# Kernel tuning notes

Measured on AMD Instinct MI355X. Metric: run time of the kernel, lower is better.

## Reference

```python
import jax, jax.numpy as jnp
import numpy as np

N = 100000   # nodes per type
E = 400000   # edges per relation
D = 128      # in_dim == out_dim
H = 4        # heads
DK = D // H  # 32
EPS = 1e-5


def setup_inputs() -> dict:
    key = jax.random.key(0)
    ks = jax.random.split(key, 16)
    s = 1.0 / np.sqrt(D)  # fan-in scaling for stable activations
    inp = {
        "x_drug": jax.random.normal(ks[0], (N, D), jnp.float32),
        "x_dis": jax.random.normal(ks[1], (N, D), jnp.float32),
        "Wp_drug": jax.random.normal(ks[2], (D, D), jnp.float32) * s,
        "bp_drug": jnp.zeros((D,), jnp.float32),
        "Wp_dis": jax.random.normal(ks[3], (D, D), jnp.float32) * s,
        "bp_dis": jnp.zeros((D,), jnp.float32),
        "Wk_r0": jax.random.normal(ks[4], (D, D), jnp.float32) * s,
        "Wv_r0": jax.random.normal(ks[5], (D, D), jnp.float32) * s,
        "Wk_r1": jax.random.normal(ks[6], (D, D), jnp.float32) * s,
        "Wv_r1": jax.random.normal(ks[7], (D, D), jnp.float32) * s,
        "Wu_drug": jax.random.normal(ks[8], (D, D), jnp.float32) * s,
        "bu_drug": jnp.zeros((D,), jnp.float32),
        "Wu_dis": jax.random.normal(ks[9], (D, D), jnp.float32) * s,
        "bu_dis": jnp.zeros((D,), jnp.float32),
        "g_drug": jnp.ones((D,), jnp.float32),
        "be_drug": jnp.zeros((D,), jnp.float32),
        "g_dis": jnp.ones((D,), jnp.float32),
        "be_dis": jnp.zeros((D,), jnp.float32),
        "ei_r0": jax.random.randint(ks[10], (2, E), 0, N, jnp.int32),  # drug -> dis
        "ei_r1": jax.random.randint(ks[11], (2, E), 0, N, jnp.int32),  # dis  -> drug
    }
    return inp


def _rel_attention(h_src_all, h_dst_all, ei, Wk, Wv, n_dst):
    # gather -> per-relation K/V proj -> edge softmax over dst -> scatter-add
    src, dst = ei[0], ei[1]
    h_src = h_src_all[src]                                  # [E, D]
    Q = h_dst_all[dst].reshape(-1, H, DK)                   # [E, H, DK]
    K = (h_src @ Wk).reshape(-1, H, DK)
    V = (h_src @ Wv).reshape(-1, H, DK)
    scores = jnp.sum(Q * K, axis=-1) / np.sqrt(DK)          # [E, H]
    # scatter_softmax over destination groups (numerically stable)
    m = jax.lax.stop_gradient(
        jax.ops.segment_max(scores, dst, num_segments=n_dst))  # [N, H]
    ex = jnp.exp(scores - m[dst])
    ssum = jax.ops.segment_sum(ex, dst, num_segments=n_dst)    # [N, H]
    attn = ex / ssum[dst]                                      # [E, H]
    wV = (V * attn[..., None]).reshape(-1, D)                  # [E, D]
    return jax.ops.segment_sum(wV, dst, num_segments=n_dst)    # [N, D]


def _update(h, agg, Wu, bu, g, be):
    x = h + (agg @ Wu + bu)  # skip + update (dropout=0)
    mu = jnp.mean(x, axis=-1, keepdims=True)
    var = jnp.var(x, axis=-1, keepdims=True)
    ln = (x - mu) * jax.lax.rsqrt(var + EPS) * g + be
    return jax.nn.relu(ln)


def reference(x_drug, x_dis, Wp_drug, bp_drug, Wp_dis, bp_dis,
              Wk_r0, Wv_r0, Wk_r1, Wv_r1,
              Wu_drug, bu_drug, Wu_dis, bu_dis,
              g_drug, be_drug, g_dis, be_dis, ei_r0, ei_r1):
    # type-specific projection
    h_drug = x_drug @ Wp_drug + bp_drug
    h_dis = x_dis @ Wp_dis + bp_dis
    # per-relation attention + intra/inter-type aggregation
    agg_dis = _rel_attention(h_drug, h_dis, ei_r0, Wk_r0, Wv_r0, N)
    agg_drug = _rel_attention(h_dis, h_drug, ei_r1, Wk_r1, Wv_r1, N)
    out_drug = _update(h_drug, agg_drug, Wu_drug, bu_drug, g_drug, be_drug)
    out_dis = _update(h_dis, agg_dis, Wu_dis, bu_dis, g_dis, be_dis)
    return jnp.stack([out_drug, out_dis])  # [2, N, D]
```

## Files before the change

kernel.cpp:

```cpp
#include <hip/hip_runtime.h>
#include <math.h>

#define NN 100000
#define EE 400000
#define DD 128

typedef __attribute__((ext_vector_type(8))) short bf16x8;
typedef __attribute__((ext_vector_type(4))) float f32x4;

__device__ __forceinline__ unsigned short f2bf(float f) {
  unsigned u = __float_as_uint(f);
  u += 0x7FFF + ((u >> 16) & 1);
  return (unsigned short)(u >> 16);
}
__device__ __forceinline__ float bf2f(unsigned short u) {
  return __uint_as_float(((unsigned)u) << 16);
}

__global__ __launch_bounds__(256) void prep_weights(
    const float* __restrict__ Wp_dr, const float* __restrict__ bp_dr,
    const float* __restrict__ Wp_di, const float* __restrict__ bp_di,
    const float* __restrict__ Wu_dr, const float* __restrict__ Wu_di,
    const float* __restrict__ Bk0, const float* __restrict__ Bv0,
    const float* __restrict__ Bk1, const float* __restrict__ Bv1,
    unsigned short* __restrict__ Wpt_dr, unsigned short* __restrict__ Wpt_di,
    unsigned short* __restrict__ Wut_dr, unsigned short* __restrict__ Wut_di,
    unsigned short* __restrict__ Wkt0, float* __restrict__ bk0,
    unsigned short* __restrict__ Wvt0, float* __restrict__ bv0,
    unsigned short* __restrict__ Wkt1, float* __restrict__ bk1,
    unsigned short* __restrict__ Wvt1, float* __restrict__ bv1) {
  const int b = blockIdx.x, t = threadIdx.x;
  if (b < 256) {
    const int id = b * 256 + t;
    const int m = id >> 14, rem = id & 16383, k = rem & 127, c = rem >> 7;
    const float* W = (m == 0) ? Wp_dr : (m == 1) ? Wp_di : (m == 2) ? Wu_dr : Wu_di;
    unsigned short* O = (m == 0) ? Wpt_dr : (m == 1) ? Wpt_di : (m == 2) ? Wut_dr : Wut_di;
    O[c * DD + k] = f2bf(W[(size_t)k * DD + c]);
  } else if (b < 512) {
    const int id = (b - 256) * 256 + t;
    const int m = id >> 14, rem = id & 16383, k = rem & 127, c = rem >> 7;
    const float* A = (m < 2) ? Wp_dr : Wp_di;
    const float* B = (m == 0) ? Bk0 : (m == 1) ? Bv0 : (m == 2) ? Bk1 : Bv1;
    unsigned short* O = (m == 0) ? Wkt0 : (m == 1) ? Wvt0 : (m == 2) ? Wkt1 : Wvt1;
    const float4* a4 = (const float4*)(A + (size_t)k * DD);
    float s = 0.0f;
#pragma unroll 8
    for (int j4 = 0; j4 < 32; ++j4) {
      const float4 av = a4[j4];
      s += av.x * B[(4 * j4 + 0) * DD + c] + av.y * B[(4 * j4 + 1) * DD + c]
         + av.z * B[(4 * j4 + 2) * DD + c] + av.w * B[(4 * j4 + 3) * DD + c];
    }
    O[c * DD + k] = f2bf(s);
  } else {
    const int id = (b - 512) * 256 + t;
    if (id < 512) {
      const int m = id >> 7, c = id & 127;
      const float* bp = (m < 2) ? bp_dr : bp_di;
      const float* B = (m == 0) ? Bk0 : (m == 1) ? Bv0 : (m == 2) ? Bk1 : Bv1;
      float* bo = (m == 0) ? bk0 : (m == 1) ? bv0 : (m == 2) ? bk1 : bv1;
      float s = 0.0f;
#pragma unroll 8
      for (int j = 0; j < DD; ++j) s += bp[j] * B[j * DD + c];
      bo[c] = s;
    }
  }
}

#define STAGE_W(SRC)                                                          \
  do {                                                                        \
    __syncthreads();                                                          \
    _Pragma("unroll") for (int i_ = threadIdx.x; i_ < 2048; i_ += 256) {      \
      const int L_ = i_ * 16;                                                 \
      *(float4*)((char*)WL + (L_ ^ (((L_ >> 8) & 7) << 4))) =                 \
          ((const float4*)(SRC))[i_];                                         \
    }                                                                         \
    __syncthreads();                                                          \
  } while (0)

__device__ __forceinline__ void mfma_tile_store(
    const unsigned short* WL, const bf16x8* a, int lane, int rowbase,
    bool wvalid, const float* __restrict__ bias, float* __restrict__ outf,
    unsigned short* __restrict__ outb) {
  const int r0 = rowbase + (lane >> 4) * 4;
#pragma unroll
  for (int ni = 0; ni < 8; ++ni) {
    const int cl = ni * 16 + (lane & 15);
    f32x4 acc = {0.f, 0.f, 0.f, 0.f};
#pragma unroll
    for (int kk = 0; kk < 4; ++kk) {
      int boff = cl * 256 + kk * 64 + (lane >> 4) * 16;
      boff ^= (cl & 7) << 4;
      const bf16x8 bb = *(const bf16x8*)((const char*)WL + boff);
      acc = __builtin_amdgcn_mfma_f32_16x16x32_bf16(a[kk], bb, acc, 0, 0, 0);
    }
    if (wvalid) {
      const float bv = bias[cl];
      if (outf) {
#pragma unroll
        for (int r = 0; r < 4; ++r)
          outf[(size_t)(r0 + r) * DD + cl] = acc[r] + bv;
      } else {
#pragma unroll
        for (int r = 0; r < 4; ++r)
          outb[(size_t)(r0 + r) * DD + cl] = f2bf(acc[r] + bv);
      }
    }
  }
}

__global__ __launch_bounds__(256) void fused_proj(
    const float* __restrict__ x0, const unsigned short* __restrict__ Wpt0,
    const float* __restrict__ bp0, const unsigned short* __restrict__ Wkta,
    const float* __restrict__ bka, const unsigned short* __restrict__ Wvta,
    const float* __restrict__ bva, float* __restrict__ h0,
    unsigned short* __restrict__ K0, unsigned short* __restrict__ V0,
    const float* __restrict__ x1, const unsigned short* __restrict__ Wpt1,
    const float* __restrict__ bp1, const unsigned short* __restrict__ Wktb,
    const float* __restrict__ bkb, const unsigned short* __restrict__ Wvtb,
    const float* __restrict__ bvb, float* __restrict__ h1,
    unsigned short* __restrict__ K1, unsigned short* __restrict__ V1, int half) {
  __shared__ unsigned short WL[DD * DD];
  int bid = blockIdx.x;
  const bool second = bid >= half;
  if (second) bid -= half;
  const float* x = second ? x1 : x0;
  const unsigned short* Wpt = second ? Wpt1 : Wpt0;
  const float* bpv = second ? bp1 : bp0;
  const unsigned short* Wkt = second ? Wktb : Wkta;
  const float* bkv = second ? bkb : bka;
  const unsigned short* Wvt = second ? Wvtb : Wvta;
  const float* bvv = second ? bvb : bva;
  float* h = second ? h1 : h0;
  unsigned short* K = second ? K1 : K0;
  unsigned short* V = second ? V1 : V0;

  const int tid = threadIdx.x, lane = tid & 63, wid = tid >> 6;
  const int rowbase = bid * 64 + wid * 16;
  const bool wvalid = rowbase < NN;
  bf16x8 a[4];
  if (wvalid) {
    const int arow = rowbase + (lane & 15);
    const float* xr = x + (size_t)arow * DD + (lane >> 4) * 8;
#pragma unroll
    for (int kk = 0; kk < 4; ++kk) {
      const float4 f0 = *(const float4*)(xr + kk * 32);
      const float4 f1 = *(const float4*)(xr + kk * 32 + 4);
      a[kk][0] = (short)f2bf(f0.x); a[kk][1] = (short)f2bf(f0.y);
      a[kk][2] = (short)f2bf(f0.z); a[kk][3] = (short)f2bf(f0.w);
      a[kk][4] = (short)f2bf(f1.x); a[kk][5] = (short)f2bf(f1.y);
      a[kk][6] = (short)f2bf(f1.z); a[kk][7] = (short)f2bf(f1.w);
    }
  } else {
#pragma unroll
    for (int kk = 0; kk < 4; ++kk)
#pragma unroll
      for (int j = 0; j < 8; ++j) a[kk][j] = 0;
  }
  STAGE_W(Wpt);
  mfma_tile_store(WL, a, lane, rowbase, wvalid, bpv, h, nullptr);
  STAGE_W(Wkt);
  mfma_tile_store(WL, a, lane, rowbase, wvalid, bkv, nullptr, K);
  STAGE_W(Wvt);
  mfma_tile_store(WL, a, lane, rowbase, wvalid, bvv, nullptr, V);
}

__global__ __launch_bounds__(256) void update_ln2(
    const float* __restrict__ ha, const unsigned short* __restrict__ agga,
    const unsigned short* __restrict__ Wuta, const float* __restrict__ bua,
    const float* __restrict__ ga, const float* __restrict__ bea,
    float* __restrict__ outa,
    const float* __restrict__ hb, const unsigned short* __restrict__ aggb,
    const unsigned short* __restrict__ Wutb, const float* __restrict__ bub,
    const float* __restrict__ gb, const float* __restrict__ beb,
    float* __restrict__ outb, int half) {
  __shared__ unsigned short WL[DD * DD];
  int bid = blockIdx.x;
  const bool second = bid >= half;
  if (second) bid -= half;
  const float* h = second ? hb : ha;
  const unsigned short* agg = second ? aggb : agga;
  const unsigned short* Wut = second ? Wutb : Wuta;
  const float* bu = second ? bub : bua;
  const float* g = second ? gb : ga;
  const float* be = second ? beb : bea;
  float* out = second ? outb : outa;

  const int tid = threadIdx.x, lane = tid & 63, wid = tid >> 6;
  const int rowbase = bid * 64 + wid * 16;
  const bool wvalid = rowbase < NN;
  bf16x8 a[4];
  if (wvalid) {
    const int arow = rowbase + (lane & 15);
#pragma unroll
    for (int kk = 0; kk < 4; ++kk)
      a[kk] = *(const bf16x8*)(agg + (size_t)arow * DD + kk * 32 + (lane >> 4) * 8);
  } else {
#pragma unroll
    for (int kk = 0; kk < 4; ++kk)
#pragma unroll
      for (int j = 0; j < 8; ++j) a[kk][j] = 0;
  }
  STAGE_W(Wut);
  f32x4 acc[8];
  const int r0 = rowbase + (lane >> 4) * 4;
#pragma unroll
  for (int ni = 0; ni < 8; ++ni) {
    const int cl = ni * 16 + (lane & 15);
    acc[ni] = (f32x4){0.f, 0.f, 0.f, 0.f};
#pragma unroll
    for (int kk = 0; kk < 4; ++kk) {
      int boff = cl * 256 + kk * 64 + (lane >> 4) * 16;
      boff ^= (cl & 7) << 4;
      const bf16x8 bb = *(const bf16x8*)((const char*)WL + boff);
      acc[ni] = __builtin_amdgcn_mfma_f32_16x16x32_bf16(a[kk], bb, acc[ni], 0, 0, 0);
    }
  }
  if (!wvalid) return;
#pragma unroll
  for (int ni = 0; ni < 8; ++ni) {
    const int cl = ni * 16 + (lane & 15);
    const float bv = bu[cl];
#pragma unroll
    for (int r = 0; r < 4; ++r)
      acc[ni][r] += h[(size_t)(r0 + r) * DD + cl] + bv;
  }
  float mean[4], inv[4];
#pragma unroll
  for (int r = 0; r < 4; ++r) {
    float s = 0.f, q = 0.f;
#pragma unroll
    for (int ni = 0; ni < 8; ++ni) {
      const float v = acc[ni][r];
      s += v; q += v * v;
    }
    s += __shfl_xor(s, 1); q += __shfl_xor(q, 1);
    s += __shfl_xor(s, 2); q += __shfl_xor(q, 2);
    s += __shfl_xor(s, 4); q += __shfl_xor(q, 4);
    s += __shfl_xor(s, 8); q += __shfl_xor(q, 8);
    const float mu = s * (1.0f / 128.0f);
    mean[r] = mu;
    inv[r] = rsqrtf(q * (1.0f / 128.0f) - mu * mu + 1e-5f);
  }
#pragma unroll
  for (int ni = 0; ni < 8; ++ni) {
    const int cl = ni * 16 + (lane & 15);
    const float gv = g[cl], bev = be[cl];
#pragma unroll
    for (int r = 0; r < 4; ++r)
      out[(size_t)(r0 + r) * DD + cl] =
          fmaxf((acc[ni][r] - mean[r]) * inv[r] * gv + bev, 0.0f);
  }
}

__global__ __launch_bounds__(256) void count_deg2(const int* __restrict__ ei0,
                                                  const int* __restrict__ ei1,
                                                  int* __restrict__ deg) {
  const int e = blockIdx.x * 256 + threadIdx.x;
  if (e >= 2 * EE) return;
  const int d = (e < EE) ? ei0[EE + e] : (NN + ei1[e]);
  atomicAdd(&deg[d], 1);
}

__global__ __launch_bounds__(256) void scan1(const int* __restrict__ deg,
                                             int* __restrict__ excl,
                                             int* __restrict__ partials, int n) {
  __shared__ int ls[256];
  const int b0 = blockIdx.x * 1024;
  const int t = threadIdx.x;
  int v[4];
  int s = 0;
#pragma unroll
  for (int i = 0; i < 4; ++i) {
    const int idx = b0 + t * 4 + i;
    v[i] = (idx < n) ? deg[idx] : 0;
    s += v[i];
  }
  ls[t] = s;
  __syncthreads();
  for (int off = 1; off < 256; off <<= 1) {
    const int x = (t >= off) ? ls[t - off] : 0;
    __syncthreads();
    ls[t] += x;
    __syncthreads();
  }
  int ex = ls[t] - s;
#pragma unroll
  for (int i = 0; i < 4; ++i) {
    const int idx = b0 + t * 4 + i;
    if (idx < n) excl[idx] = ex;
    ex += v[i];
  }
  if (t == 255) partials[blockIdx.x] = ls[255];
}

__global__ __launch_bounds__(256) void scan2(int* __restrict__ partials, int nb) {
  __shared__ int ls[256];
  const int t = threadIdx.x;
  const int v = (t < nb) ? partials[t] : 0;
  ls[t] = v;
  __syncthreads();
  for (int off = 1; off < 256; off <<= 1) {
    const int x = (t >= off) ? ls[t - off] : 0;
    __syncthreads();
    ls[t] += x;
    __syncthreads();
  }
  if (t < nb) partials[t] = ls[t] - v;
}

__global__ __launch_bounds__(256) void scan3(const int* __restrict__ excl,
                                             const int* __restrict__ partials,
                                             int n, int* __restrict__ rowptr,
                                             int* __restrict__ cursor) {
  const int i = blockIdx.x * 256 + threadIdx.x;
  if (i < n) {
    const int v = excl[i] + partials[i >> 10];
    rowptr[i] = v;
    cursor[i] = v;
  }
  if (i == 0) rowptr[n] = 2 * EE;
}

__global__ __launch_bounds__(256) void fill_csr2(const int* __restrict__ ei0,
                                                 const int* __restrict__ ei1,
                                                 int* __restrict__ cursor,
                                                 int* __restrict__ csr_src) {
  const int e = blockIdx.x * 256 + threadIdx.x;
  if (e >= 2 * EE) return;
  int s, d;
  if (e < EE) { s = ei0[e]; d = ei0[EE + e]; }
  else        { s = ei1[e - EE]; d = NN + ei1[e]; }
  const int p = atomicAdd(&cursor[d], 1);
  csr_src[p] = s;
}

__global__ __launch_bounds__(256) void dst_attention(
    const float* __restrict__ Hq0, const unsigned short* __restrict__ K0,
    const unsigned short* __restrict__ V0, unsigned short* __restrict__ agg0,
    const float* __restrict__ Hq1, const unsigned short* __restrict__ K1,
    const unsigned short* __restrict__ V1, unsigned short* __restrict__ agg1,
    const int* __restrict__ rowptr, const int* __restrict__ csr_src) {
  const int gw = blockIdx.x * 4 + (threadIdx.x >> 6);
  if (gw >= 2 * NN) return;
  const bool rel1 = gw >= NN;
  const int node = rel1 ? gw - NN : gw;
  const float* Hq = rel1 ? Hq1 : Hq0;
  const unsigned short* K = rel1 ? K1 : K0;
  const unsigned short* V = rel1 ? V1 : V0;
  unsigned short* agg = rel1 ? agg1 : agg0;

  const int lane = threadIdx.x & 63;
  const int sub = lane & 15;
  const int grp = lane >> 4;
  const int beg = rowptr[gw], end = rowptr[gw + 1];
  const float4* qp = (const float4*)(Hq + (size_t)node * DD + sub * 8);
  const float4 q0 = qp[0], q1 = qp[1];
  float av[8] = {0.f, 0.f, 0.f, 0.f, 0.f, 0.f, 0.f, 0.f};
  float lsum = 0.0f;
  for (int i = beg + grp; i < end; i += 4) {
    const int sidx = csr_src[i];
    const uint4 kp = *(const uint4*)(K + (size_t)sidx * DD + sub * 8);
    float p;
    p  = q0.x * __uint_as_float(kp.x << 16);
    p += q0.y * __uint_as_float(kp.x & 0xFFFF0000u);
    p += q0.z * __uint_as_float(kp.y << 16);
    p += q0.w * __uint_as_float(kp.y & 0xFFFF0000u);
    p += q1.x * __uint_as_float(kp.z << 16);
    p += q1.y * __uint_as_float(kp.z & 0xFFFF0000u);
    p += q1.z * __uint_as_float(kp.w << 16);
    p += q1.w * __uint_as_float(kp.w & 0xFFFF0000u);
    p += __shfl_xor(p, 1);
    p += __shfl_xor(p, 2);
    const float wgt = __expf(p * 0.17677669529663689f);
    const uint4 vp = *(const uint4*)(V + (size_t)sidx * DD + sub * 8);
    lsum += wgt;
    av[0] += wgt * __uint_as_float(vp.x << 16);
    av[1] += wgt * __uint_as_float(vp.x & 0xFFFF0000u);
    av[2] += wgt * __uint_as_float(vp.y << 16);
    av[3] += wgt * __uint_as_float(vp.y & 0xFFFF0000u);
    av[4] += wgt * __uint_as_float(vp.z << 16);
    av[5] += wgt * __uint_as_float(vp.z & 0xFFFF0000u);
    av[6] += wgt * __uint_as_float(vp.w << 16);
    av[7] += wgt * __uint_as_float(vp.w & 0xFFFF0000u);
  }
#pragma unroll
  for (int d = 0; d < 8; ++d) {
    av[d] += __shfl_xor(av[d], 16);
    av[d] += __shfl_xor(av[d], 32);
  }
  lsum += __shfl_xor(lsum, 16);
  lsum += __shfl_xor(lsum, 32);
  if (grp == 0) {
    const float invl = (lsum > 0.0f) ? (1.0f / lsum) : 0.0f;
    uint4 o;
    o.x = (unsigned)f2bf(av[0] * invl) | ((unsigned)f2bf(av[1] * invl) << 16);
    o.y = (unsigned)f2bf(av[2] * invl) | ((unsigned)f2bf(av[3] * invl) << 16);
    o.z = (unsigned)f2bf(av[4] * invl) | ((unsigned)f2bf(av[5] * invl) << 16);
    o.w = (unsigned)f2bf(av[6] * invl) | ((unsigned)f2bf(av[7] * invl) << 16);
    *(uint4*)(agg + (size_t)node * DD + sub * 8) = o;
  }
}

extern "C" void kernel_launch(void* const* d_in, const int* in_sizes, int n_in,
                              void* d_out, int out_size, void* d_ws, size_t ws_size,
                              hipStream_t stream) {
  const float* x_drug  = (const float*)d_in[0];
  const float* x_dis   = (const float*)d_in[1];
  const float* Wp_drug = (const float*)d_in[2];
  const float* bp_drug = (const float*)d_in[3];
  const float* Wp_dis  = (const float*)d_in[4];
  const float* bp_dis  = (const float*)d_in[5];
  const float* Wk_r0   = (const float*)d_in[6];
  const float* Wv_r0   = (const float*)d_in[7];
  const float* Wk_r1   = (const float*)d_in[8];
  const float* Wv_r1   = (const float*)d_in[9];
  const float* Wu_drug = (const float*)d_in[10];
  const float* bu_drug = (const float*)d_in[11];
  const float* Wu_dis  = (const float*)d_in[12];
  const float* bu_dis  = (const float*)d_in[13];
  const float* g_drug  = (const float*)d_in[14];
  const float* be_drug = (const float*)d_in[15];
  const float* g_dis   = (const float*)d_in[16];
  const float* be_dis  = (const float*)d_in[17];
  const int* ei_r0     = (const int*)d_in[18];
  const int* ei_r1     = (const int*)d_in[19];

  float* out = (float*)d_out;
  float* h_drug = out;
  float* h_dis  = out + (size_t)NN * DD;

  const size_t ND = (size_t)NN * DD;
  char* w = (char*)d_ws;
  unsigned short* Kr0  = (unsigned short*)w; w += ND * 2;
  unsigned short* Vr0  = (unsigned short*)w; w += ND * 2;
  unsigned short* Kr1  = (unsigned short*)w; w += ND * 2;
  unsigned short* Vr1  = (unsigned short*)w; w += ND * 2;
  unsigned short* agdr = (unsigned short*)w; w += ND * 2;
  unsigned short* agdi = (unsigned short*)w; w += ND * 2;
  unsigned short* Wpt_dr = (unsigned short*)w; w += DD * DD * 2;
  unsigned short* Wpt_di = (unsigned short*)w; w += DD * DD * 2;
  unsigned short* Wut_dr = (unsigned short*)w; w += DD * DD * 2;
  unsigned short* Wut_di = (unsigned short*)w; w += DD * DD * 2;
  unsigned short* Wkt0 = (unsigned short*)w; w += DD * DD * 2;
  unsigned short* Wvt0 = (unsigned short*)w; w += DD * DD * 2;
  unsigned short* Wkt1 = (unsigned short*)w; w += DD * DD * 2;
  unsigned short* Wvt1 = (unsigned short*)w; w += DD * DD * 2;
  float* bk0 = (float*)w; w += DD * 4;
  float* bv0 = (float*)w; w += DD * 4;
  float* bk1 = (float*)w; w += DD * 4;
  float* bv1 = (float*)w; w += DD * 4;
  int* deg      = (int*)w; w += 2 * NN * 4;
  int* excl     = (int*)w; w += 2 * NN * 4;
  int* rowptr   = (int*)w; w += (2 * NN + 1) * 4;
  int* cursor   = (int*)w; w += 2 * NN * 4;
  int* partials = (int*)w; w += 256 * 4;
  int* csr_src  = (int*)w; w += 2 * EE * 4;

  const int gemm_blocks = (NN + 63) / 64;
  const int edge_blocks2 = (2 * EE + 255) / 256;
  const int nchunks = (2 * NN + 1023) / 1024;
  const int n256 = (2 * NN + 255) / 256;
  const int attn_blocks = (2 * NN + 3) / 4;
  dim3 b256(256);

  prep_weights<<<514, b256, 0, stream>>>(
      Wp_drug, bp_drug, Wp_dis, bp_dis, Wu_drug, Wu_dis,
      Wk_r0, Wv_r0, Wk_r1, Wv_r1,
      Wpt_dr, Wpt_di, Wut_dr, Wut_di,
      Wkt0, bk0, Wvt0, bv0, Wkt1, bk1, Wvt1, bv1);

  fused_proj<<<2 * gemm_blocks, b256, 0, stream>>>(
      x_drug, Wpt_dr, bp_drug, Wkt0, bk0, Wvt0, bv0, h_drug, Kr0, Vr0,
      x_dis,  Wpt_di, bp_dis,  Wkt1, bk1, Wvt1, bv1, h_dis,  Kr1, Vr1,
      gemm_blocks);

  hipMemsetAsync(deg, 0, 2 * NN * sizeof(int), stream);
  count_deg2<<<edge_blocks2, b256, 0, stream>>>(ei_r0, ei_r1, deg);
  scan1<<<nchunks, b256, 0, stream>>>(deg, excl, partials, 2 * NN);
  scan2<<<1, b256, 0, stream>>>(partials, nchunks);
  scan3<<<n256, b256, 0, stream>>>(excl, partials, 2 * NN, rowptr, cursor);
  fill_csr2<<<edge_blocks2, b256, 0, stream>>>(ei_r0, ei_r1, cursor, csr_src);

  dst_attention<<<attn_blocks, b256, 0, stream>>>(
      h_dis, Kr0, Vr0, agdi,
      h_drug, Kr1, Vr1, agdr,
      rowptr, csr_src);

  update_ln2<<<2 * gemm_blocks, b256, 0, stream>>>(
      h_drug, agdr, Wut_dr, bu_drug, g_drug, be_drug, h_drug,
      h_dis,  agdi, Wut_di, bu_dis,  g_dis,  be_dis,  h_dis,
      gemm_blocks);
}
```

Before: 316.1 us.

## Store projected h in bf16 and stage GEMM tiles through LDS for coalesced I/O

The projected node features h are now written as a bf16 workspace buffer instead of fp32 in the output, which halves their write traffic and the reads made by attention and update. The GEMM kernels now stage input rows and output tiles through shared memory so global loads and stores are full-row coalesced vectors. The attention query dot product uses the bf16 fdot2 builtin when it is available. In exchange the kernels use more LDS, which may lower occupancy, and h loses precision before the residual add.

```diff
diff --git a/kernel.cpp b/kernel.cpp
--- a/kernel.cpp
+++ b/kernel.cpp
@@ -7,6 +7,13 @@
 
 typedef __attribute__((ext_vector_type(8))) short bf16x8;
 typedef __attribute__((ext_vector_type(4))) float f32x4;
+
+#if defined(__has_builtin)
+#if __has_builtin(__builtin_amdgcn_fdot2_f32_bf16)
+#define HAVE_FDOT2 1
+typedef __attribute__((ext_vector_type(2))) __bf16 bf16x2t;
+#endif
+#endif
 
 __device__ __forceinline__ unsigned short f2bf(float f) {
   unsigned u = __float_as_uint(f);
@@ -66,22 +73,19 @@
   }
 }
 
-#define STAGE_W(SRC)                                                          \
-  do {                                                                        \
-    __syncthreads();                                                          \
-    _Pragma("unroll") for (int i_ = threadIdx.x; i_ < 2048; i_ += 256) {      \
-      const int L_ = i_ * 16;                                                 \
-      *(float4*)((char*)WL + (L_ ^ (((L_ >> 8) & 7) << 4))) =                 \
-          ((const float4*)(SRC))[i_];                                         \
-    }                                                                         \
-    __syncthreads();                                                          \
-  } while (0)
-
-__device__ __forceinline__ void mfma_tile_store(
-    const unsigned short* WL, const bf16x8* a, int lane, int rowbase,
-    bool wvalid, const float* __restrict__ bias, float* __restrict__ outf,
-    unsigned short* __restrict__ outb) {
-  const int r0 = rowbase + (lane >> 4) * 4;
+__device__ __forceinline__ void proj_phase(
+    const unsigned short* __restrict__ Wt, const float* __restrict__ bias,
+    unsigned short* __restrict__ outg, unsigned short* WL, unsigned short* OT,
+    const bf16x8* a, int tid, int lane, int wid, int rb) {
+  __syncthreads();
+#pragma unroll
+  for (int i = tid; i < 2048; i += 256) {
+    const int L = i * 16;
+    *(float4*)((char*)WL + (L ^ (((L >> 8) & 7) << 4))) = ((const float4*)Wt)[i];
+  }
+  __syncthreads();
+  const int lr0 = (lane >> 4) * 4;
+  const int trow = wid * 16 + lr0;
 #pragma unroll
   for (int ni = 0; ni < 8; ++ni) {
     const int cl = ni * 16 + (lane & 15);
@@ -93,18 +97,17 @@
       const bf16x8 bb = *(const bf16x8*)((const char*)WL + boff);
       acc = __builtin_amdgcn_mfma_f32_16x16x32_bf16(a[kk], bb, acc, 0, 0, 0);
     }
-    if (wvalid) {
-      const float bv = bias[cl];
-      if (outf) {
-#pragma unroll
-        for (int r = 0; r < 4; ++r)
-          outf[(size_t)(r0 + r) * DD + cl] = acc[r] + bv;
-      } else {
-#pragma unroll
-        for (int r = 0; r < 4; ++r)
-          outb[(size_t)(r0 + r) * DD + cl] = f2bf(acc[r] + bv);
-      }
-    }
+    const float bv = bias[cl];
+#pragma unroll
+    for (int r = 0; r < 4; ++r)
+      OT[(trow + r) * DD + cl] = f2bf(acc[r] + bv);
+  }
+  __syncthreads();
+#pragma unroll
+  for (int it = 0; it < 4; ++it) {
+    const int row = it * 16 + (tid >> 4), c = (tid & 15) * 8;
+    if (rb + row < NN)
+      *(uint4*)(outg + (size_t)(rb + row) * DD + c) = *(const uint4*)(OT + row * DD + c);
   }
 }
 
@@ -112,14 +115,16 @@
     const float* __restrict__ x0, const unsigned short* __restrict__ Wpt0,
     const float* __restrict__ bp0, const unsigned short* __restrict__ Wkta,
     const float* __restrict__ bka, const unsigned short* __restrict__ Wvta,
-    const float* __restrict__ bva, float* __restrict__ h0,
+    const float* __restrict__ bva, unsigned short* __restrict__ h0,
     unsigned short* __restrict__ K0, unsigned short* __restrict__ V0,
     const float* __restrict__ x1, const unsigned short* __restrict__ Wpt1,
     const float* __restrict__ bp1, const unsigned short* __restrict__ Wktb,
     const float* __restrict__ bkb, const unsigned short* __restrict__ Wvtb,
-    const float* __restrict__ bvb, float* __restrict__ h1,
+    const float* __restrict__ bvb, unsigned short* __restrict__ h1,
     unsigned short* __restrict__ K1, unsigned short* __restrict__ V1, int half) {
   __shared__ unsigned short WL[DD * DD];
+  __shared__ unsigned short AL[64 * DD];
+  __shared__ unsigned short OT[64 * DD];
   int bid = blockIdx.x;
   const bool second = bid >= half;
   if (second) bid -= half;
@@ -130,79 +135,98 @@
   const float* bkv = second ? bkb : bka;
   const unsigned short* Wvt = second ? Wvtb : Wvta;
   const float* bvv = second ? bvb : bva;
-  float* h = second ? h1 : h0;
+  unsigned short* h = second ? h1 : h0;
   unsigned short* K = second ? K1 : K0;
   unsigned short* V = second ? V1 : V0;
 
   const int tid = threadIdx.x, lane = tid & 63, wid = tid >> 6;
-  const int rowbase = bid * 64 + wid * 16;
-  const bool wvalid = rowbase < NN;
+  const int rb = bid * 64;
+#pragma unroll
+  for (int it = 0; it < 8; ++it) {
+    const int r = it * 8 + (tid >> 5), c = (tid & 31) * 4;
+    unsigned long long pk = 0;
+    if (rb + r < NN) {
+      const float4 f = *(const float4*)(x + (size_t)(rb + r) * DD + c);
+      pk = (unsigned long long)f2bf(f.x) | ((unsigned long long)f2bf(f.y) << 16)
+         | ((unsigned long long)f2bf(f.z) << 32) | ((unsigned long long)f2bf(f.w) << 48);
+    }
+    int L = r * 256 + c * 2;
+    L ^= (r & 7) << 4;
+    *(unsigned long long*)((char*)AL + L) = pk;
+  }
+  __syncthreads();
   bf16x8 a[4];
-  if (wvalid) {
-    const int arow = rowbase + (lane & 15);
-    const float* xr = x + (size_t)arow * DD + (lane >> 4) * 8;
+  {
+    const int ar = wid * 16 + (lane & 15);
 #pragma unroll
     for (int kk = 0; kk < 4; ++kk) {
-      const float4 f0 = *(const float4*)(xr + kk * 32);
-      const float4 f1 = *(const float4*)(xr + kk * 32 + 4);
-      a[kk][0] = (short)f2bf(f0.x); a[kk][1] = (short)f2bf(f0.y);
-      a[kk][2] = (short)f2bf(f0.z); a[kk][3] = (short)f2bf(f0.w);
-      a[kk][4] = (short)f2bf(f1.x); a[kk][5] = (short)f2bf(f1.y);
-      a[kk][6] = (short)f2bf(f1.z); a[kk][7] = (short)f2bf(f1.w);
-    }
-  } else {
-#pragma unroll
-    for (int kk = 0; kk < 4; ++kk)
-#pragma unroll
-      for (int j = 0; j < 8; ++j) a[kk][j] = 0;
-  }
-  STAGE_W(Wpt);
-  mfma_tile_store(WL, a, lane, rowbase, wvalid, bpv, h, nullptr);
-  STAGE_W(Wkt);
-  mfma_tile_store(WL, a, lane, rowbase, wvalid, bkv, nullptr, K);
-  STAGE_W(Wvt);
-  mfma_tile_store(WL, a, lane, rowbase, wvalid, bvv, nullptr, V);
+      int L = ar * 256 + kk * 64 + (lane >> 4) * 16;
+      L ^= (ar & 7) << 4;
+      a[kk] = *(const bf16x8*)((const char*)AL + L);
+    }
+  }
+  proj_phase(Wpt, bpv, h, WL, OT, a, tid, lane, wid, rb);
+  proj_phase(Wkt, bkv, K, WL, OT, a, tid, lane, wid, rb);
+  proj_phase(Wvt, bvv, V, WL, OT, a, tid, lane, wid, rb);
 }
 
 __global__ __launch_bounds__(256) void update_ln2(
-    const float* __restrict__ ha, const unsigned short* __restrict__ agga,
-    const unsigned short* __restrict__ Wuta, const float* __restrict__ bua,
-    const float* __restrict__ ga, const float* __restrict__ bea,
-    float* __restrict__ outa,
-    const float* __restrict__ hb, const unsigned short* __restrict__ aggb,
-    const unsigned short* __restrict__ Wutb, const float* __restrict__ bub,
-    const float* __restrict__ gb, const float* __restrict__ beb,
-    float* __restrict__ outb, int half) {
+    const unsigned short* __restrict__ hA, const unsigned short* __restrict__ aggA,
+    const unsigned short* __restrict__ WutA, const float* __restrict__ buA,
+    const float* __restrict__ gA, const float* __restrict__ beA,
+    float* __restrict__ outA,
+    const unsigned short* __restrict__ hB, const unsigned short* __restrict__ aggB,
+    const unsigned short* __restrict__ WutB, const float* __restrict__ buB,
+    const float* __restrict__ gB, const float* __restrict__ beB,
+    float* __restrict__ outB, int half) {
   __shared__ unsigned short WL[DD * DD];
+  __shared__ unsigned short AL[64 * DD];
+  __shared__ unsigned short OT[64 * DD];
   int bid = blockIdx.x;
   const bool second = bid >= half;
   if (second) bid -= half;
-  const float* h = second ? hb : ha;
-  const unsigned short* agg = second ? aggb : agga;
-  const unsigned short* Wut = second ? Wutb : Wuta;
-  const float* bu = second ? bub : bua;
-  const float* g = second ? gb : ga;
-  const float* be = second ? beb : bea;
-  float* out = second ? outb : outa;
+  const unsigned short* h = second ? hB : hA;
+  const unsigned short* agg = second ? aggB : aggA;
+  const unsigned short* Wut = second ? WutB : WutA;
+  const float* bu = second ? buB : buA;
+  const float* g = second ? gB : gA;
+  const float* be = second ? beB : beA;
+  float* out = second ? outB : outA;
 
   const int tid = threadIdx.x, lane = tid & 63, wid = tid >> 6;
-  const int rowbase = bid * 64 + wid * 16;
-  const bool wvalid = rowbase < NN;
+  const int rb = bid * 64;
+#pragma unroll
+  for (int it = 0; it < 4; ++it) {
+    const int row = it * 16 + (tid >> 4), c = (tid & 15) * 8;
+    uint4 va = {0, 0, 0, 0}, vh = {0, 0, 0, 0};
+    if (rb + row < NN) {
+      va = *(const uint4*)(agg + (size_t)(rb + row) * DD + c);
+      vh = *(const uint4*)(h + (size_t)(rb + row) * DD + c);
+    }
+    int L = row * 256 + c * 2;
+    L ^= (row & 7) << 4;
+    *(uint4*)((char*)AL + L) = va;
+    *(uint4*)(OT + row * DD + c) = vh;
+  }
+#pragma unroll
+  for (int i = tid; i < 2048; i += 256) {
+    const int L = i * 16;
+    *(float4*)((char*)WL + (L ^ (((L >> 8) & 7) << 4))) = ((const float4*)Wut)[i];
+  }
+  __syncthreads();
   bf16x8 a[4];
-  if (wvalid) {
-    const int arow = rowbase + (lane & 15);
-#pragma unroll
-    for (int kk = 0; kk < 4; ++kk)
-      a[kk] = *(const bf16x8*)(agg + (size_t)arow * DD + kk * 32 + (lane >> 4) * 8);
-  } else {
-#pragma unroll
-    for (int kk = 0; kk < 4; ++kk)
-#pragma unroll
-      for (int j = 0; j < 8; ++j) a[kk][j] = 0;
-  }
-  STAGE_W(Wut);
+  {
+    const int ar = wid * 16 + (lane & 15);
+#pragma unroll
+    for (int kk = 0; kk < 4; ++kk) {
+      int L = ar * 256 + kk * 64 + (lane >> 4) * 16;
+      L ^= (ar & 7) << 4;
+      a[kk] = *(const bf16x8*)((const char*)AL + L);
+    }
+  }
   f32x4 acc[8];
-  const int r0 = rowbase + (lane >> 4) * 4;
+  const int lr0 = (lane >> 4) * 4;
+  const int trow = wid * 16 + lr0;
 #pragma unroll
   for (int ni = 0; ni < 8; ++ni) {
     const int cl = ni * 16 + (lane & 15);
@@ -215,14 +239,13 @@
       acc[ni] = __builtin_amdgcn_mfma_f32_16x16x32_bf16(a[kk], bb, acc[ni], 0, 0, 0);
     }
   }
-  if (!wvalid) return;
 #pragma unroll
   for (int ni = 0; ni < 8; ++ni) {
     const int cl = ni * 16 + (lane & 15);
     const float bv = bu[cl];
 #pragma unroll
     for (int r = 0; r < 4; ++r)
-      acc[ni][r] += h[(size_t)(r0 + r) * DD + cl] + bv;
+      acc[ni][r] += bf2f(OT[(trow + r) * DD + cl]) + bv;
   }
   float mean[4], inv[4];
 #pragma unroll
@@ -241,14 +264,23 @@
     mean[r] = mu;
     inv[r] = rsqrtf(q * (1.0f / 128.0f) - mu * mu + 1e-5f);
   }
+  __syncthreads();
+  float* WLf = (float*)WL;
 #pragma unroll
   for (int ni = 0; ni < 8; ++ni) {
     const int cl = ni * 16 + (lane & 15);
     const float gv = g[cl], bev = be[cl];
 #pragma unroll
     for (int r = 0; r < 4; ++r)
-      out[(size_t)(r0 + r) * DD + cl] =
+      WLf[(trow + r) * DD + cl] =
           fmaxf((acc[ni][r] - mean[r]) * inv[r] * gv + bev, 0.0f);
+  }
+  __syncthreads();
+#pragma unroll
+  for (int it = 0; it < 8; ++it) {
+    const int row = it * 8 + (tid >> 5), c = (tid & 31) * 4;
+    if (rb + row < NN)
+      *(float4*)(out + (size_t)(rb + row) * DD + c) = *(const float4*)(WLf + row * DD + c);
   }
 }
 
@@ -335,16 +367,16 @@
 }
 
 __global__ __launch_bounds__(256) void dst_attention(
-    const float* __restrict__ Hq0, const unsigned short* __restrict__ K0,
+    const unsigned short* __restrict__ Hq0, const unsigned short* __restrict__ K0,
     const unsigned short* __restrict__ V0, unsigned short* __restrict__ agg0,
-    const float* __restrict__ Hq1, const unsigned short* __restrict__ K1,
+    const unsigned short* __restrict__ Hq1, const unsigned short* __restrict__ K1,
     const unsigned short* __restrict__ V1, unsigned short* __restrict__ agg1,
     const int* __restrict__ rowptr, const int* __restrict__ csr_src) {
   const int gw = blockIdx.x * 4 + (threadIdx.x >> 6);
   if (gw >= 2 * NN) return;
   const bool rel1 = gw >= NN;
   const int node = rel1 ? gw - NN : gw;
-  const float* Hq = rel1 ? Hq1 : Hq0;
+  const unsigned short* Hq = rel1 ? Hq1 : Hq0;
   const unsigned short* K = rel1 ? K1 : K0;
   const unsigned short* V = rel1 ? V1 : V0;
   unsigned short* agg = rel1 ? agg1 : agg0;
@@ -353,22 +385,36 @@
   const int sub = lane & 15;
   const int grp = lane >> 4;
   const int beg = rowptr[gw], end = rowptr[gw + 1];
-  const float4* qp = (const float4*)(Hq + (size_t)node * DD + sub * 8);
-  const float4 q0 = qp[0], q1 = qp[1];
+  const uint4 qu = *(const uint4*)(Hq + (size_t)node * DD + sub * 8);
+#if defined(HAVE_FDOT2)
+  const bf16x2t q0 = __builtin_bit_cast(bf16x2t, qu.x);
+  const bf16x2t q1 = __builtin_bit_cast(bf16x2t, qu.y);
+  const bf16x2t q2 = __builtin_bit_cast(bf16x2t, qu.z);
+  const bf16x2t q3 = __builtin_bit_cast(bf16x2t, qu.w);
+#else
+  float qf[8];
+  qf[0] = bf2f((unsigned short)qu.x); qf[1] = bf2f((unsigned short)(qu.x >> 16));
+  qf[2] = bf2f((unsigned short)qu.y); qf[3] = bf2f((unsigned short)(qu.y >> 16));
+  qf[4] = bf2f((unsigned short)qu.z); qf[5] = bf2f((unsigned short)(qu.z >> 16));
+  qf[6] = bf2f((unsigned short)qu.w); qf[7] = bf2f((unsigned short)(qu.w >> 16));
+#endif
   float av[8] = {0.f, 0.f, 0.f, 0.f, 0.f, 0.f, 0.f, 0.f};
   float lsum = 0.0f;
   for (int i = beg + grp; i < end; i += 4) {
     const int sidx = csr_src[i];
     const uint4 kp = *(const uint4*)(K + (size_t)sidx * DD + sub * 8);
+#if defined(HAVE_FDOT2)
+    float p = __builtin_amdgcn_fdot2_f32_bf16(__builtin_bit_cast(bf16x2t, kp.x), q0, 0.0f, false);
+    p = __builtin_amdgcn_fdot2_f32_bf16(__builtin_bit_cast(bf16x2t, kp.y), q1, p, false);
+    p = __builtin_amdgcn_fdot2_f32_bf16(__builtin_bit_cast(bf16x2t, kp.z), q2, p, false);
+    p = __builtin_amdgcn_fdot2_f32_bf16(__builtin_bit_cast(bf16x2t, kp.w), q3, p, false);
+#else
     float p;
-    p  = q0.x * __uint_as_float(kp.x << 16);
-    p += q0.y * __uint_as_float(kp.x & 0xFFFF0000u);
-    p += q0.z * __uint_as_float(kp.y << 16);
-    p += q0.w * __uint_as_float(kp.y & 0xFFFF0000u);
-    p += q1.x * __uint_as_float(kp.z << 16);
-    p += q1.y * __uint_as_float(kp.z & 0xFFFF0000u);
-    p += q1.z * __uint_as_float(kp.w << 16);
-    p += q1.w * __uint_as_float(kp.w & 0xFFFF0000u);
+    p  = qf[0] * bf2f((unsigned short)kp.x) + qf[1] * bf2f((unsigned short)(kp.x >> 16));
+    p += qf[2] * bf2f((unsigned short)kp.y) + qf[3] * bf2f((unsigned short)(kp.y >> 16));
+    p += qf[4] * bf2f((unsigned short)kp.z) + qf[5] * bf2f((unsigned short)(kp.z >> 16));
+    p += qf[6] * bf2f((unsigned short)kp.w) + qf[7] * bf2f((unsigned short)(kp.w >> 16));
+#endif
     p += __shfl_xor(p, 1);
     p += __shfl_xor(p, 2);
     const float wgt = __expf(p * 0.17677669529663689f);
@@ -426,8 +472,8 @@
   const int* ei_r1     = (const int*)d_in[19];
 
   float* out = (float*)d_out;
-  float* h_drug = out;
-  float* h_dis  = out + (size_t)NN * DD;
+  float* out_drug = out;
+  float* out_dis  = out + (size_t)NN * DD;
 
   const size_t ND = (size_t)NN * DD;
   char* w = (char*)d_ws;
@@ -437,6 +483,8 @@
   unsigned short* Vr1  = (unsigned short*)w; w += ND * 2;
   unsigned short* agdr = (unsigned short*)w; w += ND * 2;
   unsigned short* agdi = (unsigned short*)w; w += ND * 2;
+  unsigned short* hb_dr = (unsigned short*)w; w += ND * 2;
+  unsigned short* hb_di = (unsigned short*)w; w += ND * 2;
   unsigned short* Wpt_dr = (unsigned short*)w; w += DD * DD * 2;
   unsigned short* Wpt_di = (unsigned short*)w; w += DD * DD * 2;
   unsigned short* Wut_dr = (unsigned short*)w; w += DD * DD * 2;
@@ -470,8 +518,8 @@
       Wkt0, bk0, Wvt0, bv0, Wkt1, bk1, Wvt1, bv1);
 
   fused_proj<<<2 * gemm_blocks, b256, 0, stream>>>(
-      x_drug, Wpt_dr, bp_drug, Wkt0, bk0, Wvt0, bv0, h_drug, Kr0, Vr0,
-      x_dis,  Wpt_di, bp_dis,  Wkt1, bk1, Wvt1, bv1, h_dis,  Kr1, Vr1,
+      x_drug, Wpt_dr, bp_drug, Wkt0, bk0, Wvt0, bv0, hb_dr, Kr0, Vr0,
+      x_dis,  Wpt_di, bp_dis,  Wkt1, bk1, Wvt1, bv1, hb_di, Kr1, Vr1,
       gemm_blocks);
 
   hipMemsetAsync(deg, 0, 2 * NN * sizeof(int), stream);
@@ -482,12 +530,12 @@
   fill_csr2<<<edge_blocks2, b256, 0, stream>>>(ei_r0, ei_r1, cursor, csr_src);
 
   dst_attention<<<attn_blocks, b256, 0, stream>>>(
-      h_dis, Kr0, Vr0, agdi,
-      h_drug, Kr1, Vr1, agdr,
+      hb_di, Kr0, Vr0, agdi,
+      hb_dr, Kr1, Vr1, agdr,
       rowptr, csr_src);
 
   update_ln2<<<2 * gemm_blocks, b256, 0, stream>>>(
-      h_drug, agdr, Wut_dr, bu_drug, g_drug, be_drug, h_drug,
-      h_dis,  agdi, Wut_di, bu_dis,  g_dis,  be_dis,  h_dis,
+      hb_dr, agdr, Wut_dr, bu_drug, g_drug, be_drug, out_drug,
+      hb_di, agdi, Wut_di, bu_dis,  g_dis,  be_dis,  out_dis,
       gemm_blocks);
 }
```

New measurement: 345.8 us. +9.4%, slower.
